# Kernel tuning notes

Measured on AMD Instinct MI355X. Metric: run time of the kernel, lower is better.

## Reference

```python
import jax, jax.numpy as jnp
import numpy as np

B, S, D = 2, 2048, 1024
H = 16
DH = D // H  # 64


def setup_inputs() -> dict:
    key = jax.random.key(0)
    k1, k2, k3 = jax.random.split(key, 3)
    X = jax.random.normal(k1, (B, S, D), dtype=jnp.float32)
    # xavier_normal for Linear(D, 3*D): std = sqrt(2/(fan_in+fan_out))
    std_qkv = float(np.sqrt(2.0 / (D + 3 * D)))
    std_out = float(np.sqrt(2.0 / (D + D)))
    W_qkv = jax.random.normal(k2, (3 * H * DH, D), dtype=jnp.float32) * std_qkv
    W_out = jax.random.normal(k3, (D, H * DH), dtype=jnp.float32) * std_out
    return {"X": X, "W_qkv": W_qkv, "W_out": W_out}


def reference(X, W_qkv, W_out):
    b, s, d = X.shape
    # stacked projection: (b, s, 3*H*DH), then per-head chunk into q,k,v
    qkv = jnp.einsum('bsd,ed->bse', X, W_qkv)
    qkv = qkv.reshape(b, s, H, 3 * DH)
    q, k, v = jnp.split(qkv, 3, axis=-1)  # each (b, s, H, DH)
    scale = 1.0 / jnp.sqrt(jnp.asarray(DH, dtype=X.dtype))
    # naive unfused attention: full [b,H,s,s] score matrix
    scores = jnp.einsum('bqhd,bkhd->bhqk', q, k) * scale
    attn = jax.nn.softmax(scores, axis=-1)
    vals = jnp.einsum('bhqk,bkhd->bqhd', attn, v)
    vals = vals.reshape(b, s, H * DH)
    out = jnp.einsum('bse,de->bsd', vals, W_out)
    return out
```

## Files before the change

kernel.cpp:

```cpp
#include <hip/hip_runtime.h>
#include <cstdint>
#include <cstddef>

typedef __bf16 bf16;
typedef __bf16 bf16x8 __attribute__((ext_vector_type(8)));
typedef __bf16 bf16x2 __attribute__((ext_vector_type(2)));
typedef float  floatx4 __attribute__((ext_vector_type(4)));

typedef __attribute__((address_space(1))) void gvoid_t;
typedef __attribute__((address_space(3))) void lvoid_t;

#define MFMA16(a, b, c) __builtin_amdgcn_mfma_f32_16x16x32_bf16((a), (b), (c), 0, 0, 0)

#if __has_builtin(__builtin_amdgcn_exp2f)
#define EXP2(x) __builtin_amdgcn_exp2f(x)
#else
#define EXP2(x) exp2f(x)
#endif

#define S_TOK 2048
#define E3 3072
#define DMODEL 1024

__global__ __launch_bounds__(256) void cvt_f32_bf16(const float* __restrict__ s,
                                                    bf16* __restrict__ d, int n) {
  int i = (blockIdx.x * 256 + threadIdx.x) * 8;
  if (i >= n) return;
  const float4* p = (const float4*)(s + i);
  float4 a = p[0], b = p[1];
  bf16x8 o;
  o[0] = (bf16)a.x; o[1] = (bf16)a.y; o[2] = (bf16)a.z; o[3] = (bf16)a.w;
  o[4] = (bf16)b.x; o[5] = (bf16)b.y; o[6] = (bf16)b.z; o[7] = (bf16)b.w;
  *(bf16x8*)(d + i) = o;
}

__global__ __launch_bounds__(256) void cvt_wqkv(const float* __restrict__ s,
                                                bf16* __restrict__ d, int n) {
  int i = (blockIdx.x * 256 + threadIdx.x) * 8;
  if (i >= n) return;
  int row = i >> 10;
  float sc = ((row % 192) < 64) ? 0.18033688011f : 1.0f;
  const float4* p = (const float4*)(s + i);
  float4 a = p[0], b = p[1];
  bf16x8 o;
  o[0] = (bf16)(a.x * sc); o[1] = (bf16)(a.y * sc);
  o[2] = (bf16)(a.z * sc); o[3] = (bf16)(a.w * sc);
  o[4] = (bf16)(b.x * sc); o[5] = (bf16)(b.y * sc);
  o[6] = (bf16)(b.z * sc); o[7] = (bf16)(b.w * sc);
  *(bf16x8*)(d + i) = o;
}

__device__ __forceinline__ void gl_lds16(const bf16* g, bf16* l) {
  __builtin_amdgcn_global_load_lds((gvoid_t*)g, (lvoid_t*)l, 16, 0, 0);
}

template <bool OUT_BF16>
__global__ __launch_bounds__(256) void gemm_bt(const bf16* __restrict__ A,
                                               const bf16* __restrict__ Bt,
                                               void* __restrict__ Cv,
                                               int M, int N, int K) {
  __shared__ bf16 sA[128 * 32];
  __shared__ bf16 sB[128 * 32];
  const int tid = threadIdx.x;
  const int wv = tid >> 6, lane = tid & 63;
  const int wr = wv >> 1, wc = wv & 1;
  const int lrow = lane & 15, lgrp = lane >> 4;
  const int R0 = blockIdx.y * 128, C0 = blockIdx.x * 128;

  floatx4 acc[4][4] = {};

  const bf16* gA = A + (size_t)(R0 + wv * 32 + (lane >> 2)) * K + (lane & 3) * 8;
  const bf16* gB = Bt + (size_t)(C0 + wv * 32 + (lane >> 2)) * K + (lane & 3) * 8;
  bf16* lA = sA + wv * 1024;
  bf16* lB = sB + wv * 1024;
  const size_t rowstep = (size_t)16 * K;

  for (int k0 = 0; k0 < K; k0 += 32) {
    gl_lds16(gA + k0, lA);
    gl_lds16(gA + k0 + rowstep, lA + 512);
    gl_lds16(gB + k0, lB);
    gl_lds16(gB + k0 + rowstep, lB + 512);
    __syncthreads();
    bf16x8 af[4], bfr[4];
#pragma unroll
    for (int i = 0; i < 4; i++)
      af[i] = *(const bf16x8*)&sA[(wr * 64 + i * 16 + lrow) * 32 + lgrp * 8];
#pragma unroll
    for (int j = 0; j < 4; j++)
      bfr[j] = *(const bf16x8*)&sB[(wc * 64 + j * 16 + lrow) * 32 + lgrp * 8];
#pragma unroll
    for (int i = 0; i < 4; i++)
#pragma unroll
      for (int j = 0; j < 4; j++)
        acc[i][j] = MFMA16(af[i], bfr[j], acc[i][j]);
    __syncthreads();
  }

  const int rbase = R0 + wr * 64 + lgrp * 4;
  const int cbase = C0 + wc * 64 + lrow;
  if (OUT_BF16) {
    bf16* C = (bf16*)Cv;
#pragma unroll
    for (int i = 0; i < 4; i++)
#pragma unroll
      for (int j = 0; j < 4; j++)
#pragma unroll
        for (int r = 0; r < 4; r++)
          C[(size_t)(rbase + i * 16 + r) * N + cbase + j * 16] = (bf16)acc[i][j][r];
  } else {
    float* C = (float*)Cv;
#pragma unroll
    for (int i = 0; i < 4; i++)
#pragma unroll
      for (int j = 0; j < 4; j++)
#pragma unroll
        for (int r = 0; r < 4; r++)
          C[(size_t)(rbase + i * 16 + r) * N + cbase + j * 16] = acc[i][j][r];
  }
}

__global__ __launch_bounds__(256) void transpose_v(const bf16* __restrict__ qkv,
                                                   bf16* __restrict__ Vt) {
  __shared__ bf16 sT[64 * 72];
  const int tid = threadIdx.x;
  const int b = blockIdx.z, h = blockIdx.y, s0 = blockIdx.x * 64;
  const bf16* vsrc = qkv + (size_t)(b * S_TOK + s0) * E3 + h * 192 + 128;
#pragma unroll
  for (int j = 0; j < 8; j++) {
    int idx = tid + 256 * j;
    int sl = idx & 63, dp = idx >> 6;
    unsigned u = *(const unsigned*)(vsrc + (size_t)sl * E3 + 2 * dp);
    sT[(2 * dp) * 72 + sl] = __builtin_bit_cast(bf16, (unsigned short)(u & 0xffffu));
    sT[(2 * dp + 1) * 72 + sl] = __builtin_bit_cast(bf16, (unsigned short)(u >> 16));
  }
  __syncthreads();
  bf16* vdst = Vt + ((size_t)(b * 16 + h) * 64) * S_TOK + s0;
#pragma unroll
  for (int j = 0; j < 2; j++) {
    int idx = tid + 256 * j;
    int d = idx >> 3, sc8 = (idx & 7) * 8;
    bf16x8 o;
#pragma unroll
    for (int m2 = 0; m2 < 8; m2++) {
      int sp = sc8 + m2;
      int ss = (sp & ~31) | ((sp >> 1) & 15) | ((sp & 1) << 4);
      o[m2] = sT[d * 72 + ss];
    }
    *(bf16x8*)(vdst + (size_t)d * S_TOK + sc8) = o;
  }
}

__global__ __launch_bounds__(256, 3) void attn(const bf16* __restrict__ qkv,
                                               const bf16* __restrict__ Vt,
                                               bf16* __restrict__ vals) {
  __shared__ bf16 sK[2][64 * 64];
  __shared__ bf16 sV[2][64 * 64];
  __shared__ bf16 sP[4][2][16 * 40];

  const int tid = threadIdx.x;
  const int wv = tid >> 6, lane = tid & 63;
  const int lrow = lane & 15, lgrp = lane >> 4;
  const int b = blockIdx.z, h = blockIdx.y;
  const int qb = blockIdx.x * 128;

  const int srow = lane >> 3;
  const int scol = (lane & 7) ^ srow;
  const bf16* kg0 = qkv + (size_t)(b * S_TOK + wv * 16 + srow) * E3 + h * 192 + 64 + scol * 8;
  const bf16* vg0 = Vt + (size_t)((b * 16 + h) * 64 + wv * 16 + srow) * S_TOK + scol * 8;

  const bf16* qp = qkv + (size_t)(b * S_TOK + qb + wv * 32) * E3 + h * 192;
  bf16x8 qa[2][2];
#pragma unroll
  for (int rt = 0; rt < 2; rt++)
#pragma unroll
    for (int dh = 0; dh < 2; dh++)
      qa[rt][dh] = *(const bf16x8*)(qp + (size_t)(rt * 16 + lrow) * E3 + dh * 32 + lgrp * 8);

  floatx4 O[2][4] = {};
  floatx4 lacc[2] = {};
  bf16x8 ones;
  const bf16 one1 = (bf16)1.0f;
#pragma unroll
  for (int j = 0; j < 8; j++) ones[j] = one1;

  const int xsw = (lrow & 7);

  auto stage = [&](int buf, int kt) {
    const bf16* kg = kg0 + (size_t)kt * 64 * E3;
    gl_lds16(kg, &sK[buf][wv * 1024]);
    gl_lds16(kg + (size_t)8 * E3, &sK[buf][wv * 1024 + 512]);
    const bf16* vg = vg0 + kt * 64;
    gl_lds16(vg, &sV[buf][wv * 1024]);
    gl_lds16(vg + 8 * S_TOK, &sV[buf][wv * 1024 + 512]);
  };

  auto compute = [&](int buf) {
#pragma unroll
    for (int g = 0; g < 2; g++) {
      bf16x8 kf[2][2];
#pragma unroll
      for (int t = 0; t < 2; t++)
#pragma unroll
        for (int dh = 0; dh < 2; dh++)
          kf[t][dh] = *(const bf16x8*)&sK[buf][(g * 32 + t * 16 + lrow) * 64 +
                                              ((dh * 4 + lgrp) ^ xsw) * 8];
#pragma unroll
      for (int rt = 0; rt < 2; rt++) {
        floatx4 sc0 = {0.f, 0.f, 0.f, 0.f}, sc1 = {0.f, 0.f, 0.f, 0.f};
        sc0 = MFMA16(qa[rt][0], kf[0][0], sc0);
        sc0 = MFMA16(qa[rt][1], kf[0][1], sc0);
        sc1 = MFMA16(qa[rt][0], kf[1][0], sc1);
        sc1 = MFMA16(qa[rt][1], kf[1][1], sc1);
#pragma unroll
        for (int r = 0; r < 4; r++) {
          bf16x2 h2;
          h2[0] = (bf16)EXP2(sc0[r]);
          h2[1] = (bf16)EXP2(sc1[r]);
          *(unsigned*)&sP[wv][rt][(lgrp * 4 + r) * 40 + lrow * 2] =
              __builtin_bit_cast(unsigned, h2);
        }
      }
      bf16x8 vf[4];
#pragma unroll
      for (int dt = 0; dt < 4; dt++)
        vf[dt] = *(const bf16x8*)&sV[buf][(dt * 16 + lrow) * 64 +
                                          ((g * 4 + lgrp) ^ xsw) * 8];
#pragma unroll
      for (int rt = 0; rt < 2; rt++) {
        bf16x8 pf = *(const bf16x8*)&sP[wv][rt][lrow * 40 + lgrp * 8];
#pragma unroll
        for (int dt = 0; dt < 4; dt++) O[rt][dt] = MFMA16(pf, vf[dt], O[rt][dt]);
        lacc[rt] = MFMA16(pf, ones, lacc[rt]);
      }
    }
  };

  stage(0, 0);
  __syncthreads();
#pragma unroll 1
  for (int kt = 0; kt < 32; kt += 2) {
    stage(1, kt + 1);
    compute(0);
    __syncthreads();
    if (kt + 2 < 32) stage(0, kt + 2);
    compute(1);
    __syncthreads();
  }

  bf16* vout = vals + (size_t)(b * S_TOK + qb + wv * 32) * DMODEL + h * 64;
#pragma unroll
  for (int rt = 0; rt < 2; rt++)
#pragma unroll
    for (int r = 0; r < 4; r++) {
      float rinv = __builtin_amdgcn_rcpf(lacc[rt][r]);
#pragma unroll
      for (int dt = 0; dt < 4; dt++)
        vout[(size_t)(rt * 16 + lgrp * 4 + r) * DMODEL + dt * 16 + lrow] =
            (bf16)(O[rt][dt][r] * rinv);
    }
}

extern "C" void kernel_launch(void* const* d_in, const int* in_sizes, int n_in,
                              void* d_out, int out_size, void* d_ws, size_t ws_size,
                              hipStream_t stream) {
  const float* X = (const float*)d_in[0];
  const float* Wqkv = (const float*)d_in[1];
  const float* Wout = (const float*)d_in[2];
  float* out = (float*)d_out;

  char* ws = (char*)d_ws;
  bf16* Xb = (bf16*)(ws);
  bf16* Wqb = (bf16*)(ws + ((size_t)8 << 20));
  bf16* Wob = (bf16*)(ws + ((size_t)14 << 20));
  bf16* qkvb = (bf16*)(ws + ((size_t)16 << 20));
  bf16* Vt = (bf16*)(ws + ((size_t)40 << 20));
  bf16* vals = (bf16*)(ws + ((size_t)48 << 20));

  cvt_f32_bf16<<<4194304 / 2048, 256, 0, stream>>>(X, Xb, 4194304);
  cvt_wqkv<<<3145728 / 2048, 256, 0, stream>>>(Wqkv, Wqb, 3145728);
  cvt_f32_bf16<<<1048576 / 2048, 256, 0, stream>>>(Wout, Wob, 1048576);

  gemm_bt<true><<<dim3(24, 32), 256, 0, stream>>>(Xb, Wqb, qkvb, 4096, 3072, 1024);

  transpose_v<<<dim3(32, 16, 2), 256, 0, stream>>>(qkvb, Vt);

  attn<<<dim3(16, 16, 2), 256, 0, stream>>>(qkvb, Vt, vals);

  gemm_bt<false><<<dim3(8, 32), 256, 0, stream>>>(vals, Wob, out, 4096, 1024, 1024);
}
```

Baseline: 202.9 us.

## Merge conversion kernels and deepen GEMM K-tile with XOR-swizzled LDS

The three f32-to-bf16 conversion launches become a single kernel that picks its source and destination by index range, which removes two kernel launches. The GEMM K-tile doubles from 32 to 64, halving the number of barrier pairs per K loop. LDS layout now uses an XOR swizzle of 16-byte chunks by row, intended to avoid bank conflicts on fragment reads. LDS use per block doubles, and loads are still not double-buffered.

```diff
diff --git a/kernel.cpp b/kernel.cpp
--- a/kernel.cpp
+++ b/kernel.cpp
@@ -22,32 +22,37 @@
 #define E3 3072
 #define DMODEL 1024
 
-__global__ __launch_bounds__(256) void cvt_f32_bf16(const float* __restrict__ s,
-                                                    bf16* __restrict__ d, int n) {
+#define NX 4194304
+#define NWQ 3145728
+#define NWO 1048576
+__global__ __launch_bounds__(256) void cvt_all(const float* __restrict__ X,
+                                               const float* __restrict__ Wq,
+                                               const float* __restrict__ Wo,
+                                               bf16* __restrict__ Xb,
+                                               bf16* __restrict__ Wqb,
+                                               bf16* __restrict__ Wob) {
   int i = (blockIdx.x * 256 + threadIdx.x) * 8;
-  if (i >= n) return;
-  const float4* p = (const float4*)(s + i);
-  float4 a = p[0], b = p[1];
-  bf16x8 o;
-  o[0] = (bf16)a.x; o[1] = (bf16)a.y; o[2] = (bf16)a.z; o[3] = (bf16)a.w;
-  o[4] = (bf16)b.x; o[5] = (bf16)b.y; o[6] = (bf16)b.z; o[7] = (bf16)b.w;
-  *(bf16x8*)(d + i) = o;
-}
-
-__global__ __launch_bounds__(256) void cvt_wqkv(const float* __restrict__ s,
-                                                bf16* __restrict__ d, int n) {
-  int i = (blockIdx.x * 256 + threadIdx.x) * 8;
-  if (i >= n) return;
-  int row = i >> 10;
-  float sc = ((row % 192) < 64) ? 0.18033688011f : 1.0f;
-  const float4* p = (const float4*)(s + i);
+  const float* s;
+  bf16* d;
+  float sc = 1.0f;
+  int off;
+  if (i < NX) {
+    s = X; d = Xb; off = i;
+  } else if (i < NX + NWQ) {
+    off = i - NX; s = Wq; d = Wqb;
+    int row = off >> 10;
+    if ((row % 192) < 64) sc = 0.18033688011f;
+  } else {
+    off = i - NX - NWQ; s = Wo; d = Wob;
+  }
+  const float4* p = (const float4*)(s + off);
   float4 a = p[0], b = p[1];
   bf16x8 o;
   o[0] = (bf16)(a.x * sc); o[1] = (bf16)(a.y * sc);
   o[2] = (bf16)(a.z * sc); o[3] = (bf16)(a.w * sc);
   o[4] = (bf16)(b.x * sc); o[5] = (bf16)(b.y * sc);
   o[6] = (bf16)(b.z * sc); o[7] = (bf16)(b.w * sc);
-  *(bf16x8*)(d + i) = o;
+  *(bf16x8*)(d + off) = o;
 }
 
 __device__ __forceinline__ void gl_lds16(const bf16* g, bf16* l) {
@@ -59,8 +64,8 @@
                                                const bf16* __restrict__ Bt,
                                                void* __restrict__ Cv,
                                                int M, int N, int K) {
-  __shared__ bf16 sA[128 * 32];
-  __shared__ bf16 sB[128 * 32];
+  __shared__ bf16 sA[128 * 64];
+  __shared__ bf16 sB[128 * 64];
   const int tid = threadIdx.x;
   const int wv = tid >> 6, lane = tid & 63;
   const int wr = wv >> 1, wc = wv & 1;
@@ -69,30 +74,40 @@
 
   floatx4 acc[4][4] = {};
 
-  const bf16* gA = A + (size_t)(R0 + wv * 32 + (lane >> 2)) * K + (lane & 3) * 8;
-  const bf16* gB = Bt + (size_t)(C0 + wv * 32 + (lane >> 2)) * K + (lane & 3) * 8;
-  bf16* lA = sA + wv * 1024;
-  bf16* lB = sB + wv * 1024;
-  const size_t rowstep = (size_t)16 * K;
-
-  for (int k0 = 0; k0 < K; k0 += 32) {
-    gl_lds16(gA + k0, lA);
-    gl_lds16(gA + k0 + rowstep, lA + 512);
-    gl_lds16(gB + k0, lB);
-    gl_lds16(gB + k0 + rowstep, lB + 512);
+  const int srow = lane >> 3;
+  const int schk = (lane & 7) ^ srow;
+  const bf16* gA = A + (size_t)(R0 + wv * 32 + srow) * K + schk * 8;
+  const bf16* gB = Bt + (size_t)(C0 + wv * 32 + srow) * K + schk * 8;
+  bf16* lA = sA + wv * 32 * 64;
+  bf16* lB = sB + wv * 32 * 64;
+  const size_t rs8 = (size_t)8 * K;
+
+  for (int k0 = 0; k0 < K; k0 += 64) {
+#pragma unroll
+    for (int c = 0; c < 4; c++) {
+      gl_lds16(gA + k0 + c * rs8, lA + c * 512);
+      gl_lds16(gB + k0 + c * rs8, lB + c * 512);
+    }
     __syncthreads();
-    bf16x8 af[4], bfr[4];
-#pragma unroll
-    for (int i = 0; i < 4; i++)
-      af[i] = *(const bf16x8*)&sA[(wr * 64 + i * 16 + lrow) * 32 + lgrp * 8];
-#pragma unroll
-    for (int j = 0; j < 4; j++)
-      bfr[j] = *(const bf16x8*)&sB[(wc * 64 + j * 16 + lrow) * 32 + lgrp * 8];
-#pragma unroll
-    for (int i = 0; i < 4; i++)
-#pragma unroll
-      for (int j = 0; j < 4; j++)
-        acc[i][j] = MFMA16(af[i], bfr[j], acc[i][j]);
+#pragma unroll
+    for (int kk = 0; kk < 2; kk++) {
+      bf16x8 af[4], bfr[4];
+#pragma unroll
+      for (int i = 0; i < 4; i++) {
+        int r = wr * 64 + i * 16 + lrow;
+        af[i] = *(const bf16x8*)&sA[r * 64 + ((kk * 4 + lgrp) ^ (r & 7)) * 8];
+      }
+#pragma unroll
+      for (int j = 0; j < 4; j++) {
+        int r = wc * 64 + j * 16 + lrow;
+        bfr[j] = *(const bf16x8*)&sB[r * 64 + ((kk * 4 + lgrp) ^ (r & 7)) * 8];
+      }
+#pragma unroll
+      for (int i = 0; i < 4; i++)
+#pragma unroll
+        for (int j = 0; j < 4; j++)
+          acc[i][j] = MFMA16(af[i], bfr[j], acc[i][j]);
+    }
     __syncthreads();
   }
 
@@ -276,9 +291,7 @@
   bf16* Vt = (bf16*)(ws + ((size_t)40 << 20));
   bf16* vals = (bf16*)(ws + ((size_t)48 << 20));
 
-  cvt_f32_bf16<<<4194304 / 2048, 256, 0, stream>>>(X, Xb, 4194304);
-  cvt_wqkv<<<3145728 / 2048, 256, 0, stream>>>(Wqkv, Wqb, 3145728);
-  cvt_f32_bf16<<<1048576 / 2048, 256, 0, stream>>>(Wout, Wob, 1048576);
+  cvt_all<<<(NX + NWQ + NWO) / 2048, 256, 0, stream>>>(X, Wqkv, Wout, Xb, Wqb, Wob);
 
   gemm_bt<true><<<dim3(24, 32), 256, 0, stream>>>(Xb, Wqb, qkvb, 4096, 3072, 1024);
 
```

Result: faster. 186.9 us (-7.9%).
